# Optimization experiments

Hardware: AMD Instinct MI355X
Metric: run time of the kernel (lower is better)

The kernel has to match this reference:

```python
import jax, jax.numpy as jnp
import numpy as np

D = 256; HEADS = 8; DH = 32; LVLS = 3; PTS = 4; FF = 1024; FCD = 12544
SHAPES = ((100, 152), (50, 76), (25, 38))  # stride 8/16/32 maps for an 800x1216 image
INCH = (512, 1024, 2048)
N = 2; P_IMG = 1000


def sine_pos(h, w):
    # PositionEmbeddingSine, normalize=True, fully-valid mask
    eps = 1e-6; scale = 2.0 * np.pi
    y = jnp.cumsum(jnp.ones((h, w), jnp.float32), 0)
    x = jnp.cumsum(jnp.ones((h, w), jnp.float32), 1)
    y = y / (y[-1:, :] + eps) * scale
    x = x / (x[:, -1:] + eps) * scale
    dim_t = 10000.0 ** ((2.0 * (jnp.arange(128) // 2)).astype(jnp.float32) / 128.0)
    def inter(p):  # interleave sin/cos like torch.stack(...).flatten(3)
        return jnp.stack([jnp.sin(p[..., 0::2]), jnp.cos(p[..., 1::2])], -1).reshape(h, w, 128)
    return jnp.concatenate([inter(y[..., None] / dim_t), inter(x[..., None] / dim_t)], -1).reshape(h * w, D)


def bilinear(img, gx, gy):
    # F.grid_sample bilinear, align_corners=False, padding_mode='zeros'
    # img [C,H,W]; gx,gy in [-1,1] of any shape -> out [C, *gx.shape]
    C, H, W = img.shape
    x = ((gx + 1.0) * W - 1.0) * 0.5
    y = ((gy + 1.0) * H - 1.0) * 0.5
    x0 = jnp.floor(x); y0 = jnp.floor(y)
    wx = x - x0; wy = y - y0
    x0i = x0.astype(jnp.int32); y0i = y0.astype(jnp.int32)
    def g(xi, yi):
        ok = ((xi >= 0) & (xi < W) & (yi >= 0) & (yi < H)).astype(img.dtype)
        v = img[:, jnp.clip(yi, 0, H - 1), jnp.clip(xi, 0, W - 1)]
        return v * ok[None]
    return (g(x0i, y0i) * ((1 - wx) * (1 - wy))[None]
            + g(x0i + 1, y0i) * (wx * (1 - wy))[None]
            + g(x0i, y0i + 1) * ((1 - wx) * wy)[None]
            + g(x0i + 1, y0i + 1) * (wx * wy)[None])


def layernorm(x, g, b):
    mu = x.mean(-1, keepdims=True)
    var = ((x - mu) ** 2).mean(-1, keepdims=True)
    return (x - mu) / jnp.sqrt(var + 1e-5) * g + b


def _forward(feat0, feat1, feat2, point_coords, projw, projb, gng, gnb, level_embed,
             w_off, b_off, w_attn, b_attn, w_val, b_val, w_out, b_out,
             ln1_g, ln1_b, ln2_g, ln2_b, w_ff1, b_ff1, w_ff2, b_ff2, fc_w, fc_b):
    feats = (feat0, feat1, feat2)
    srcs = []; poss = []
    for l in range(LVLS):
        # input_proj: 1x1 conv + GroupNorm(32, 256)
        s = jnp.einsum('nchw,oc->nohw', feats[l], projw[l]) + projb[l][None, :, None, None]
        n, c, h, w = s.shape
        sg = s.reshape(n, 32, c // 32, h, w)
        mu = sg.mean((2, 3, 4), keepdims=True)
        var = ((sg - mu) ** 2).mean((2, 3, 4), keepdims=True)
        s = ((sg - mu) / jnp.sqrt(var + 1e-5)).reshape(n, c, h, w) * gng[l][None, :, None, None] + gnb[l][None, :, None, None]
        srcs.append(s.reshape(n, c, h * w).transpose(0, 2, 1))
        poss.append(sine_pos(h, w)[None] + level_embed[l][None, None, :])
    src = jnp.concatenate(srcs, 1)            # [N, Len, D]
    pos = jnp.concatenate(poss, 1)            # [1, Len, D] broadcast
    # reference points (valid_ratios == 1)
    refs = []
    for (h, w) in SHAPES:
        gy, gx = jnp.meshgrid((jnp.arange(h) + 0.5) / h, (jnp.arange(w) + 0.5) / w, indexing='ij')
        refs.append(jnp.stack([gx.ravel(), gy.ravel()], -1))
    ref = jnp.concatenate(refs, 0)            # [Len, 2] (x, y)
    Lq = src.shape[1]
    q = src + pos
    value = (src @ w_val.T + b_val).reshape(N, Lq, HEADS, DH)
    off = (q @ w_off.T + b_off).reshape(N, Lq, HEADS, LVLS, PTS, 2)
    aw = jax.nn.softmax((q @ w_attn.T + b_attn).reshape(N, Lq, HEADS, LVLS * PTS), -1).reshape(N, Lq, HEADS, LVLS, PTS)
    norm = jnp.array([[w, h] for (h, w) in SHAPES], jnp.float32)  # [L, 2] offset normalizer (W_, H_)
    locs = ref[None, :, None, None, None, :] + off / norm[None, None, None, :, None, :]  # [N,Lq,H,L,P,2]
    # MSDeformAttn core: per-level bilinear gather, accumulate weighted samples
    acc = jnp.zeros((N * HEADS, DH, Lq), src.dtype)
    start = 0
    for lvl, (h, w) in enumerate(SHAPES):
        v = value[:, start:start + h * w].transpose(0, 2, 3, 1).reshape(N * HEADS, DH, h, w)
        g = (2.0 * locs[:, :, :, lvl] - 1.0).transpose(0, 2, 1, 3, 4).reshape(N * HEADS, Lq, PTS, 2)
        s = jax.vmap(bilinear)(v, g[..., 0], g[..., 1])                 # [NH, DH, Lq, PTS]
        a = aw[:, :, :, lvl].transpose(0, 2, 1, 3).reshape(N * HEADS, 1, Lq, PTS)
        acc = acc + (s * a).sum(-1)
        start += h * w
    attn_out = acc.reshape(N, HEADS * DH, Lq).transpose(0, 2, 1) @ w_out.T + b_out
    x = layernorm(src + attn_out, ln1_g, ln1_b)
    ff = jax.nn.relu(x @ w_ff1.T + b_ff1) @ w_ff2.T + b_ff2
    x = layernorm(x + ff, ln2_g, ln2_b)
    # take level-0 tokens back to a feature map
    H0, W0 = SHAPES[0]
    mem = x.transpose(0, 2, 1)[:, :, :H0 * W0].reshape(N, D, H0, W0)
    # point_sample: grid_sample at 2*coords-1
    gpc = 2.0 * point_coords - 1.0
    pf = jax.vmap(bilinear)(mem, gpc[..., 0], gpc[..., 1])              # [N, D, P]
    pf = pf.transpose(0, 2, 1).reshape(N * P_IMG, D)
    # fc: Conv1d(256 -> 12544, k=1) + relu, then squeeze/permute
    return jax.nn.relu(pf @ fc_w.T + fc_b[None])


def setup_inputs() -> dict:
    key = jax.random.key(0)
    ki = iter(jax.random.split(key, 48))
    def rn(shape, scale):
        return jax.random.normal(next(ki), shape, jnp.float32) * scale
    d = {}
    d['feat0'] = jax.random.normal(next(ki), (N, 512, 100, 152), jnp.float32)
    d['feat1'] = jax.random.normal(next(ki), (N, 1024, 50, 76), jnp.float32)
    d['feat2'] = jax.random.normal(next(ki), (N, 2048, 25, 38), jnp.float32)
    d['point_coords'] = jax.random.uniform(next(ki), (N, P_IMG, 2), jnp.float32)
    d['gt_classes'] = jax.random.randint(next(ki), (N * P_IMG,), 0, 81)
    for l in range(LVLS):
        cin = INCH[l]
        d[f'proj{l}_w'] = rn((D, cin), 1.0 / np.sqrt(cin))
        d[f'proj{l}_b'] = jnp.zeros((D,), jnp.float32)
        d[f'gn{l}_g'] = jnp.ones((D,), jnp.float32)
        d[f'gn{l}_b'] = jnp.zeros((D,), jnp.float32)
    d['level_embed'] = rn((LVLS, D), 1.0)
    d['w_off'] = rn((HEADS * LVLS * PTS * 2, D), 0.01)
    d['b_off'] = rn((HEADS * LVLS * PTS * 2,), 0.2)
    d['w_attn'] = rn((HEADS * LVLS * PTS, D), 0.01)
    d['b_attn'] = jnp.zeros((HEADS * LVLS * PTS,), jnp.float32)
    d['w_val'] = rn((D, D), 1.0 / 16)
    d['b_val'] = jnp.zeros((D,), jnp.float32)
    d['w_out'] = rn((D, D), 1.0 / 16)
    d['b_out'] = jnp.zeros((D,), jnp.float32)
    d['ln1_g'] = jnp.ones((D,), jnp.float32); d['ln1_b'] = jnp.zeros((D,), jnp.float32)
    d['ln2_g'] = jnp.ones((D,), jnp.float32); d['ln2_b'] = jnp.zeros((D,), jnp.float32)
    d['w_ff1'] = rn((FF, D), 1.0 / 16); d['b_ff1'] = jnp.zeros((FF,), jnp.float32)
    d['w_ff2'] = rn((D, FF), 1.0 / 32); d['b_ff2'] = jnp.zeros((D,), jnp.float32)
    d['fc_w'] = rn((FCD, D), 1.0 / 16); d['fc_b'] = jnp.zeros((FCD,), jnp.float32)
    return d


def reference(feat0, feat1, feat2, point_coords, gt_classes,
              proj0_w, proj0_b, gn0_g, gn0_b, proj1_w, proj1_b, gn1_g, gn1_b,
              proj2_w, proj2_b, gn2_g, gn2_b, level_embed,
              w_off, b_off, w_attn, b_attn, w_val, b_val, w_out, b_out,
              ln1_g, ln1_b, ln2_g, ln2_b, w_ff1, b_ff1, w_ff2, b_ff2, fc_w, fc_b):
    out = _forward(feat0, feat1, feat2, point_coords,
                   (proj0_w, proj1_w, proj2_w), (proj0_b, proj1_b, proj2_b),
                   (gn0_g, gn1_g, gn2_g), (gn0_b, gn1_b, gn2_b), level_embed,
                   w_off, b_off, w_attn, b_attn, w_val, b_val, w_out, b_out,
                   ln1_g, ln1_b, ln2_g, ln2_b, w_ff1, b_ff1, w_ff2, b_ff2, fc_w, fc_b)
    return (out, gt_classes)
```

## Files before the change

kernel.cpp:

```cpp
#include <hip/hip_runtime.h>
#include <cstddef>
#include <cstdint>

#define D_MODEL 256
#define LQ 19950
#define NBATCH 2
#define NT (NBATCH*LQ)

typedef short  bf16x8 __attribute__((ext_vector_type(8)));
typedef float  f32x4  __attribute__((ext_vector_type(4)));
typedef unsigned short u16x8 __attribute__((ext_vector_type(8)));
typedef unsigned short u16x4 __attribute__((ext_vector_type(4)));
typedef _Float16 h16x2 __attribute__((ext_vector_type(2)));

__device__ __forceinline__ unsigned short f2b(float f) {
  unsigned u = __float_as_uint(f);
  u += 0x7fff + ((u >> 16) & 1);
  return (unsigned short)(u >> 16);
}
__device__ __forceinline__ float b2f(unsigned short s) {
  return __uint_as_float(((unsigned)s) << 16);
}
__device__ __forceinline__ bf16x8 pack8(float4 a, float4 b) {
  bf16x8 r;
  r[0]=(short)f2b(a.x); r[1]=(short)f2b(a.y); r[2]=(short)f2b(a.z); r[3]=(short)f2b(a.w);
  r[4]=(short)f2b(b.x); r[5]=(short)f2b(b.y); r[6]=(short)f2b(b.z); r[7]=(short)f2b(b.w);
  return r;
}

#if __has_builtin(__builtin_amdgcn_global_load_lds)
#define HAVE_GLL 1
__device__ __forceinline__ void gload16(const void* g, void* lds_base_uniform) {
  __builtin_amdgcn_global_load_lds(
      (const __attribute__((address_space(1))) void*)g,
      (__attribute__((address_space(3))) void*)lds_base_uniform, 16, 0, 0);
}
#else
#define HAVE_GLL 0
#endif

template<bool ABF, int BMODE, bool CBF, bool RELU, bool ROWBIAS>
__global__ __launch_bounds__(256) void mgemm(
    const void* __restrict__ Av, const void* __restrict__ Bv,
    const float* __restrict__ bias, void* __restrict__ Cv,
    int M, int N, int K, int lda, int ldb, long sB, long sC, int zShift)
{
  __shared__ unsigned short As[64][72];
  __shared__ unsigned short Bs[64][72];
  const int tid = threadIdx.x;
  const int n0 = blockIdx.x * 64, m0 = blockIdx.y * 64;
  const int zb = blockIdx.z;
  const int n_b = zb >> zShift;
  const int kBase = (zb & ((1 << zShift) - 1)) * K;
  const int lane = tid & 63;
  const int wave = tid >> 6;
  const int l15 = lane & 15, q = lane >> 4;
  const int m_off = (wave >> 1) * 32, n_off = (wave & 1) * 32;
  f32x4 acc[2][2] = {};

  for (int k0 = kBase; k0 < kBase + K; k0 += 64) {
    {
      int row = tid >> 2, kc = (tid & 3) * 8;
      int gm = m0 + row;
      bf16x8 v0 = (bf16x8)0, v1 = (bf16x8)0;
      if (gm < M) {
        if constexpr (ABF) {
          const unsigned short* A = (const unsigned short*)Av;
          v0 = *(const bf16x8*)&A[(size_t)gm*lda + k0 + kc];
          v1 = *(const bf16x8*)&A[(size_t)gm*lda + k0 + kc + 32];
        } else {
          const float* A = (const float*)Av;
          const float* p = &A[(size_t)gm*lda + k0 + kc];
          v0 = pack8(*(const float4*)p,      *(const float4*)(p+4));
          v1 = pack8(*(const float4*)(p+32), *(const float4*)(p+36));
        }
      }
      *(bf16x8*)&As[row][kc]    = v0;
      *(bf16x8*)&As[row][kc+32] = v1;
    }
    if constexpr (BMODE == 1) {
      const float* Bp = (const float*)Bv + (size_t)n_b * sB;
      int kr = tid >> 3, nc = (tid & 7) * 8;
      #pragma unroll
      for (int half = 0; half < 2; ++half) {
        int kk = kr + half*32;
        const float* p = &Bp[(size_t)(k0+kk)*ldb + n0 + nc];
        float v[8];
        if (n0 + nc + 7 < N) {
          float2 a0 = *(const float2*)p,     a1 = *(const float2*)(p+2);
          float2 a2 = *(const float2*)(p+4), a3 = *(const float2*)(p+6);
          v[0]=a0.x; v[1]=a0.y; v[2]=a1.x; v[3]=a1.y;
          v[4]=a2.x; v[5]=a2.y; v[6]=a3.x; v[7]=a3.y;
        } else {
          #pragma unroll
          for (int i=0;i<8;++i) v[i] = (n0+nc+i < N) ? p[i] : 0.f;
        }
        #pragma unroll
        for (int i=0;i<8;++i) Bs[nc+i][kk] = f2b(v[i]);
      }
    }
    __syncthreads();
    #pragma unroll
    for (int s = 0; s < 2; ++s) {
      bf16x8 a0 = *(const bf16x8*)&As[m_off      + l15][s*32 + q*8];
      bf16x8 a1 = *(const bf16x8*)&As[m_off + 16 + l15][s*32 + q*8];
      bf16x8 b0 = *(const bf16x8*)&Bs[n_off      + l15][s*32 + q*8];
      bf16x8 b1 = *(const bf16x8*)&Bs[n_off + 16 + l15][s*32 + q*8];
      acc[0][0] = __builtin_amdgcn_mfma_f32_16x16x32_bf16(a0, b0, acc[0][0], 0,0,0);
      acc[0][1] = __builtin_amdgcn_mfma_f32_16x16x32_bf16(a0, b1, acc[0][1], 0,0,0);
      acc[1][0] = __builtin_amdgcn_mfma_f32_16x16x32_bf16(a1, b0, acc[1][0], 0,0,0);
      acc[1][1] = __builtin_amdgcn_mfma_f32_16x16x32_bf16(a1, b1, acc[1][1], 0,0,0);
    }
    __syncthreads();
  }
  float* Cf = (float*)Cv + (size_t)zb * sC;
  unsigned short* Cb = (unsigned short*)Cv + (size_t)zb * sC;
  #pragma unroll
  for (int r = 0; r < 2; ++r) {
    #pragma unroll
    for (int c = 0; c < 2; ++c) {
      #pragma unroll
      for (int v = 0; v < 4; ++v) {
        int gm = m0 + m_off + r*16 + q*4 + v;
        int gn = n0 + n_off + c*16 + l15;
        if (gm < M && gn < N) {
          float o = acc[r][c][v];
          if (bias) o += ROWBIAS ? bias[gm] : bias[gn];
          if (RELU) o = fmaxf(o, 0.f);
          if constexpr (CBF) Cb[(size_t)gm*N + gn] = f2b(o);
          else               Cf[(size_t)gm*N + gn] = o;
        }
      }
    }
  }
}

__global__ __launch_bounds__(256) void proj_reduce2(
    const float* __restrict__ part, const float* __restrict__ bias,
    float* __restrict__ out, int HW, int S)
{
  int half = HW >> 1;
  int per_n = D_MODEL * half;
  int total = NBATCH * per_n;
  const float2* p2 = (const float2*)part;
  float2* o2 = (float2*)out;
  for (int i = blockIdx.x*256 + threadIdx.x; i < total; i += gridDim.x*256) {
    int n = i / per_n;
    int r = i - n*per_n;
    int o = r / half;
    int hw2 = r - o*half;
    float ax = 0.f, ay = 0.f;
    for (int s = 0; s < S; ++s) {
      float2 v = p2[((size_t)(n*S+s)*D_MODEL + o)*half + hw2];
      ax += v.x; ay += v.y;
    }
    float b = bias[o];
    o2[(size_t)o*HW + (size_t)n*half + hw2] = make_float2(ax+b, ay+b);
  }
}

template<bool CBF, bool RELU, bool RB>
__global__ __launch_bounds__(512) void gemm_bb(
    const unsigned short* __restrict__ A, const unsigned short* __restrict__ B,
    const float* __restrict__ bias, void* __restrict__ Cv,
    int M, int N, int K, int lda, int ldb)
{
  __shared__ unsigned short SA[8192];
  __shared__ unsigned short SB[8192];
  const int tid = threadIdx.x;
  const int lane = tid & 63, wave = tid >> 6;
  const int nwg = gridDim.x * gridDim.y;
  const int flat = blockIdx.y * gridDim.x + blockIdx.x;
  const int qn = nwg >> 3, rr = nwg & 7;
  const int xcd = flat & 7, lid = flat >> 3;
  const int swz = (xcd < rr ? xcd*(qn+1) : rr*(qn+1) + (xcd-rr)*qn) + lid;
  const int n0 = (swz % gridDim.x) * 128;
  const int m0 = (swz / gridDim.x) * 128;

  const int l15 = lane & 15, q = lane >> 4;
  const int m_off = (wave >> 2) * 64, n_off = (wave & 3) * 32;
  const int sr = lane >> 3;
  const int ssl = (lane & 7) ^ sr;
  const int rs = l15 & 7;
  f32x4 acc[4][2] = {};

  for (int k0 = 0; k0 < K; k0 += 64) {
    #pragma unroll
    for (int c = 0; c < 2; ++c) {
      int ch = wave*2 + c;
      const unsigned short* ga = A + (size_t)(m0 + ch*8 + sr)*lda + k0 + ssl*8;
      const unsigned short* gb = B + (size_t)(n0 + ch*8 + sr)*ldb + k0 + ssl*8;
#if HAVE_GLL
      gload16(ga, &SA[ch*512]);
      gload16(gb, &SB[ch*512]);
#else
      *(bf16x8*)&SA[ch*512 + lane*8] = *(const bf16x8*)ga;
      *(bf16x8*)&SB[ch*512 + lane*8] = *(const bf16x8*)gb;
#endif
    }
    __syncthreads();
    #pragma unroll
    for (int s = 0; s < 2; ++s) {
      int ps = ((s*4 + q) ^ rs) * 8;
      bf16x8 af[4], bfr[2];
      #pragma unroll
      for (int i = 0; i < 4; ++i)
        af[i] = *(const bf16x8*)&SA[(m_off + i*16 + l15)*64 + ps];
      #pragma unroll
      for (int j = 0; j < 2; ++j)
        bfr[j] = *(const bf16x8*)&SB[(n_off + j*16 + l15)*64 + ps];
      #pragma unroll
      for (int i = 0; i < 4; ++i)
        #pragma unroll
        for (int j = 0; j < 2; ++j)
          acc[i][j] = __builtin_amdgcn_mfma_f32_16x16x32_bf16(af[i], bfr[j], acc[i][j], 0,0,0);
    }
    __syncthreads();
  }

  float* Cf = (float*)Cv;
  unsigned short* Cb = (unsigned short*)Cv;
  #pragma unroll
  for (int i = 0; i < 4; ++i) {
    #pragma unroll
    for (int j = 0; j < 2; ++j) {
      #pragma unroll
      for (int v = 0; v < 4; ++v) {
        int gm = m0 + m_off + i*16 + q*4 + v;
        int gn = n0 + n_off + j*16 + l15;
        if (gm < M && gn < N) {
          float o = acc[i][j][v];
          if (bias) o += RB ? bias[gm] : bias[gn];
          if (RELU) o = fmaxf(o, 0.f);
          if constexpr (CBF) Cb[(size_t)gm*N + gn] = f2b(o);
          else               Cf[(size_t)gm*N + gn] = o;
        }
      }
    }
  }
}

__global__ __launch_bounds__(512) void gemm_vo(
    const unsigned short* __restrict__ Asrc, const unsigned short* __restrict__ Aq,
    const unsigned short* __restrict__ Bv,   const unsigned short* __restrict__ Bo,
    const float* __restrict__ bias_v, const float* __restrict__ bias_o,
    unsigned short* __restrict__ Cv, unsigned short* __restrict__ Co, int M)
{
  __shared__ unsigned short SA[8192];
  __shared__ unsigned short SB[8192];
  const int tid = threadIdx.x;
  const int lane = tid & 63, wave = tid >> 6;
  const int nwg = gridDim.x * gridDim.y;
  const int flat = blockIdx.y * gridDim.x + blockIdx.x;
  const int qn = nwg >> 3, rr = nwg & 7;
  const int xcd = flat & 7, lid = flat >> 3;
  const int swz = (xcd < rr ? xcd*(qn+1) : rr*(qn+1) + (xcd-rr)*qn) + lid;
  const int colid = swz % gridDim.x;
  const int m0 = (swz / gridDim.x) * 128;

  const unsigned short* A; const unsigned short* B;
  const float* bias; unsigned short* C; int N, n0; bool isv;
  if (colid < 2) { A = Asrc; B = Bv; bias = bias_v; C = Cv; N = 256; n0 = colid*128; isv = true; }
  else           { A = Aq;   B = Bo; bias = bias_o; C = Co; N = 288; n0 = (colid-2)*128; isv = false; }

  const int l15 = lane & 15, q = lane >> 4;
  const int m_off = (wave >> 2) * 64, n_off = (wave & 3) * 32;
  const int sr = lane >> 3;
  const int ssl = (lane & 7) ^ sr;
  const int rs = l15 & 7;
  f32x4 acc[4][2] = {};

  for (int k0 = 0; k0 < 256; k0 += 64) {
    #pragma unroll
    for (int c = 0; c < 2; ++c) {
      int ch = wave*2 + c;
      const unsigned short* ga = A + (size_t)(m0 + ch*8 + sr)*256 + k0 + ssl*8;
      const unsigned short* gb = B + (size_t)(n0 + ch*8 + sr)*256 + k0 + ssl*8;
#if HAVE_GLL
      gload16(ga, &SA[ch*512]);
      gload16(gb, &SB[ch*512]);
#else
      *(bf16x8*)&SA[ch*512 + lane*8] = *(const bf16x8*)ga;
      *(bf16x8*)&SB[ch*512 + lane*8] = *(const bf16x8*)gb;
#endif
    }
    __syncthreads();
    #pragma unroll
    for (int s = 0; s < 2; ++s) {
      int ps = ((s*4 + q) ^ rs) * 8;
      bf16x8 af[4], bfr[2];
      #pragma unroll
      for (int i = 0; i < 4; ++i)
        af[i] = *(const bf16x8*)&SA[(m_off + i*16 + l15)*64 + ps];
      #pragma unroll
      for (int j = 0; j < 2; ++j)
        bfr[j] = *(const bf16x8*)&SB[(n_off + j*16 + l15)*64 + ps];
      #pragma unroll
      for (int i = 0; i < 4; ++i)
        #pragma unroll
        for (int j = 0; j < 2; ++j)
          acc[i][j] = __builtin_amdgcn_mfma_f32_16x16x32_bf16(af[i], bfr[j], acc[i][j], 0,0,0);
    }
    __syncthreads();
  }

  #pragma unroll
  for (int i = 0; i < 4; ++i) {
    #pragma unroll
    for (int j = 0; j < 2; ++j) {
      #pragma unroll
      for (int v = 0; v < 4; ++v) {
        int gm = m0 + m_off + i*16 + q*4 + v;
        int gn = n0 + n_off + j*16 + l15;
        if (gm < M && gn < N) {
          float o = acc[i][j][v] + bias[gn];
          unsigned short bits;
          if (isv) { _Float16 hh = (_Float16)o; bits = *(unsigned short*)&hh; }
          else     { bits = f2b(o); }
          C[(size_t)gm*N + gn] = bits;
        }
      }
    }
  }
}

__global__ __launch_bounds__(256) void tconv(
    const float* __restrict__ feat, unsigned short* __restrict__ featT,
    int C, int HW)
{
  __shared__ float T[32][33];
  int hw0 = blockIdx.x*32, c0 = blockIdx.y*32, n = blockIdx.z;
  const float* base = feat + (size_t)n*C*HW;
  int tx = threadIdx.x & 31, ty = threadIdx.x >> 5;
  #pragma unroll
  for (int it=0; it<4; ++it) {
    int c = c0 + ty + it*8;
    int hw = hw0 + tx;
    T[ty+it*8][tx] = (hw < HW) ? base[(size_t)c*HW + hw] : 0.f;
  }
  __syncthreads();
  #pragma unroll
  for (int it=0; it<4; ++it) {
    int tl = ty + it*8;
    int tok = hw0 + tl;
    if (tok < HW) {
      featT[((size_t)n*HW + tok)*C + c0 + tx] = f2b(T[tx][tl]);
    }
  }
}

struct W9 { const float* src[9]; unsigned short* dst[9]; int nv[9]; };
__global__ __launch_bounds__(256) void wconv(W9 w)
{
  int s = blockIdx.y;
  const float4* src = (const float4*)w.src[s];
  unsigned short* dst = w.dst[s];
  int n = w.nv[s];
  for (int i = blockIdx.x*256 + threadIdx.x; i < n; i += gridDim.x*256) {
    float4 v = src[i];
    u16x4 o = { f2b(v.x), f2b(v.y), f2b(v.z), f2b(v.w) };
    *(u16x4*)(dst + (size_t)i*4) = o;
  }
}

__global__ __launch_bounds__(288) void biascat(
    const float* __restrict__ b_off, const float* __restrict__ b_attn,
    float* __restrict__ out)
{
  int i = threadIdx.x;
  out[i] = (i < 192) ? b_off[i] : b_attn[i - 192];
}

__global__ __launch_bounds__(256) void gn_partial2(
    const float* __restrict__ s2, float* __restrict__ partials, int HW)
{
  int g = blockIdx.x, n = blockIdx.y, c = blockIdx.z;
  int NHW = HW*2;
  int nvec2 = HW >> 1;
  int total = nvec2*8;
  float sum = 0.f, sq = 0.f;
  for (int j = c*256 + threadIdx.x; j < total; j += 2048) {
    int r = j / nvec2;
    int v = j - r*nvec2;
    const float2 x = *(const float2*)(s2 + (size_t)(g*8+r)*NHW + (size_t)n*HW + v*2);
    sum += x.x + x.y;
    sq  += x.x*x.x + x.y*x.y;
  }
  #pragma unroll
  for (int m=32;m;m>>=1){ sum += __shfl_xor(sum,m,64); sq += __shfl_xor(sq,m,64); }
  __shared__ float s1[4], s2s[4];
  int w = threadIdx.x >> 6;
  if ((threadIdx.x & 63) == 0) { s1[w]=sum; s2s[w]=sq; }
  __syncthreads();
  if (threadIdx.x == 0) {
    partials[(((size_t)n*32+g)*8 + c)*2]     = s1[0]+s1[1]+s1[2]+s1[3];
    partials[(((size_t)n*32+g)*8 + c)*2 + 1] = s2s[0]+s2s[1]+s2s[2]+s2s[3];
  }
}

__global__ __launch_bounds__(256) void gn_apply2(
    const float* __restrict__ s2, const float* __restrict__ partials,
    const float* __restrict__ gw, const float* __restrict__ gb,
    float* __restrict__ src, int HW, int loff)
{
  __shared__ float T[32][33];
  __shared__ float smu[4], srs[4];
  int tx = threadIdx.x & 31, ty = threadIdx.x >> 5;
  int hw0 = blockIdx.x*32, o0 = blockIdx.y*32, n = blockIdx.z;
  int NHW = HW*2;
  if (threadIdx.x < 4) {
    int g = (o0 >> 3) + threadIdx.x;
    float S = 0.f, Q = 0.f;
    #pragma unroll
    for (int c = 0; c < 8; ++c) {
      S += partials[(((size_t)n*32+g)*8 + c)*2];
      Q += partials[(((size_t)n*32+g)*8 + c)*2 + 1];
    }
    float inv = 1.f/(float)(8*HW);
    float mu = S*inv;
    float var = Q*inv - mu*mu;
    smu[threadIdx.x] = mu;
    srs[threadIdx.x] = rsqrtf(var + 1e-5f);
  }
  __syncthreads();
  #pragma unroll
  for (int it=0; it<4; ++it) {
    int ol = ty + it*8;
    int o = o0 + ol;
    int hw = hw0 + tx;
    float v = 0.f;
    if (hw < HW) {
      v = (s2[(size_t)o*NHW + (size_t)n*HW + hw] - smu[ol>>3])*srs[ol>>3]*gw[o] + gb[o];
    }
    T[ol][tx] = v;
  }
  __syncthreads();
  #pragma unroll
  for (int it=0; it<4; ++it) {
    int tl = ty + it*8;
    int tok = hw0 + tl;
    if (tok < HW) {
      src[((size_t)n*LQ + loff + tok)*D_MODEL + o0 + tx] = T[tx][tl];
    }
  }
}

__global__ __launch_bounds__(256) void compute_q(
    const float* __restrict__ src, const float* __restrict__ level_embed,
    unsigned short* __restrict__ q, unsigned short* __restrict__ srcbf)
{
  int row = blockIdx.x;
  int d = threadIdx.x;
  int tok = (row >= LQ) ? row - LQ : row;
  int H, W, lvl, i, j;
  if (tok < 15200)      { lvl=0; H=100; W=152; int hw=tok;        i=hw/152; j=hw-i*152; }
  else if (tok < 19000) { lvl=1; H=50;  W=76;  int hw=tok-15200;  i=hw/76;  j=hw-i*76;  }
  else                  { lvl=2; H=25;  W=38;  int hw=tok-19000;  i=hw/38;  j=hw-i*38;  }
  const float TWO_PI = 6.28318530717958647692f;
  float yv = (float)(i+1) / ((float)H + 1e-6f) * TWO_PI;
  float xv = (float)(j+1) / ((float)W + 1e-6f) * TWO_PI;
  int m = (d & 127) >> 1;
  float invt = __expf((float)m * -0.14391156516f);
  float ang = ((d < 128) ? yv : xv) * invt;
  float pe = (d & 1) ? __cosf(ang) : __sinf(ang);
  size_t idx = (size_t)row*D_MODEL + d;
  float sv = src[idx];
  q[idx] = f2b(sv + pe + level_embed[lvl*D_MODEL + d]);
  srcbf[idx] = f2b(sv);
}

__global__ __launch_bounds__(256) void deform_sample(
    const unsigned short* __restrict__ value, const unsigned short* __restrict__ offaw,
    unsigned short* __restrict__ accb)
{
  int idx = blockIdx.x*256 + threadIdx.x;
  if (idx >= NT*8*4) return;
  int quarter = idx & 3;
  int h = (idx >> 2) & 7;
  int row = idx >> 5;
  int n = (row >= LQ) ? 1 : 0;
  int tok = row - n*LQ;

  float bxs0, bxs1, bxs2, bys0, bys1, bys2;
  if (tok < 15200) {
    int ti = tok/152, tj = tok - ti*152;
    float bx = tj + 0.5f, by = ti + 0.5f;
    bxs0 = bx - 0.5f;         bys0 = by - 0.5f;
    bxs1 = bx*0.5f - 0.5f;    bys1 = by*0.5f - 0.5f;
    bxs2 = bx*0.25f - 0.5f;   bys2 = by*0.25f - 0.5f;
  } else if (tok < 19000) {
    int hw = tok - 15200; int ti = hw/76, tj = hw - ti*76;
    float bx = tj + 0.5f, by = ti + 0.5f;
    bxs0 = bx*2.f - 0.5f;     bys0 = by*2.f - 0.5f;
    bxs1 = bx - 0.5f;         bys1 = by - 0.5f;
    bxs2 = bx*0.5f - 0.5f;    bys2 = by*0.5f - 0.5f;
  } else {
    int hw = tok - 19000; int ti = hw/38, tj = hw - ti*38;
    float bx = tj + 0.5f, by = ti + 0.5f;
    bxs0 = bx*4.f - 0.5f;     bys0 = by*4.f - 0.5f;
    bxs1 = bx*2.f - 0.5f;     bys1 = by*2.f - 0.5f;
    bxs2 = bx - 0.5f;         bys2 = by - 0.5f;
  }
  const float bxs[3] = {bxs0, bxs1, bxs2};
  const float bys[3] = {bys0, bys1, bys2};

  const unsigned short* offr = offaw + (size_t)row*288 + h*24;
  const unsigned short* awr  = offaw + (size_t)row*288 + 192 + h*12;
  float off[24];
  {
    u16x8 o0 = *(const u16x8*)offr;
    u16x8 o1 = *(const u16x8*)(offr+8);
    u16x8 o2 = *(const u16x8*)(offr+16);
    #pragma unroll
    for (int c=0;c<8;++c){ off[c]=b2f(o0[c]); off[8+c]=b2f(o1[c]); off[16+c]=b2f(o2[c]); }
  }
  float lg[12];
  {
    u16x4 a0 = *(const u16x4*)awr;
    u16x4 a1 = *(const u16x4*)(awr+4);
    u16x4 a2 = *(const u16x4*)(awr+8);
    #pragma unroll
    for (int c=0;c<4;++c){ lg[c]=b2f(a0[c]); lg[4+c]=b2f(a1[c]); lg[8+c]=b2f(a2[c]); }
  }
  float mx = -1e30f;
  #pragma unroll
  for (int i=0;i<12;++i) mx = fmaxf(mx, lg[i]);
  float ssum = 0.f;
  #pragma unroll
  for (int i=0;i<12;++i){ lg[i] = __expf(lg[i]-mx); ssum += lg[i]; }
  float sinv = 1.f/ssum;

  h16x2 acc2[4] = {};
  const int HH[3]={100,50,25}, WW[3]={152,76,38}, OO[3]={0,15200,19000};
  int chbase = h*32 + quarter*8;
  const _Float16* vhalf = (const _Float16*)value;
  #pragma unroll
  for (int lvl=0; lvl<3; ++lvl) {
    const int H=HH[lvl], W=WW[lvl], lo=OO[lvl];
    const _Float16* vbase = vhalf + ((size_t)(n*LQ + lo)*D_MODEL) + chbase;
    #pragma unroll
    for (int p=0; p<4; ++p) {
      float ox = off[lvl*8 + p*2];
      float oy = off[lvl*8 + p*2 + 1];
      float a  = lg[lvl*4 + p] * sinv;
      float x = bxs[lvl] + ox;
      float y = bys[lvl] + oy;
      float x0f = floorf(x), y0f = floorf(y);
      float wx = x - x0f, wy = y - y0f;
      int x0 = (int)x0f, y0 = (int)y0f;
      float w00 = (1.f-wx)*(1.f-wy)*a, w10 = wx*(1.f-wy)*a;
      float w01 = (1.f-wx)*wy*a,       w11 = wx*wy*a;
      if ((unsigned)x0 < (unsigned)(W-1) && (unsigned)y0 < (unsigned)(H-1)) {
        const h16x2* p00 = (const h16x2*)(vbase + (size_t)(y0*W + x0)*D_MODEL);
        const h16x2* p10 = (const h16x2*)(vbase + (size_t)(y0*W + x0 + 1)*D_MODEL);
        const h16x2* p01 = (const h16x2*)(vbase + (size_t)((y0+1)*W + x0)*D_MODEL);
        const h16x2* p11 = (const h16x2*)(vbase + (size_t)((y0+1)*W + x0 + 1)*D_MODEL);
        _Float16 h00 = (_Float16)w00, h10 = (_Float16)w10;
        _Float16 h01 = (_Float16)w01, h11 = (_Float16)w11;
        h16x2 wp00 = {h00,h00}, wp10 = {h10,h10}, wp01 = {h01,h01}, wp11 = {h11,h11};
        #pragma unroll
        for (int k=0;k<4;++k) {
          acc2[k] += wp00*p00[k];
          acc2[k] += wp10*p10[k];
          acc2[k] += wp01*p01[k];
          acc2[k] += wp11*p11[k];
        }
      } else {
        float tw[4] = { w00, w10, w01, w11 };
        #pragma unroll
        for (int t=0; t<4; ++t) {
          int xi = x0 + (t & 1), yi = y0 + (t >> 1);
          if (xi >= 0 && xi < W && yi >= 0 && yi < H) {
            _Float16 wh = (_Float16)tw[t];
            h16x2 wp = {wh, wh};
            const h16x2* vr = (const h16x2*)(vbase + (size_t)(yi*W + xi)*D_MODEL);
            #pragma unroll
            for (int k=0;k<4;++k) acc2[k] += wp*vr[k];
          }
        }
      }
    }
  }
  unsigned short* o = accb + (size_t)row*D_MODEL + chbase;
  u16x8 ov;
  #pragma unroll
  for (int k=0;k<4;++k) {
    ov[k*2]   = f2b((float)acc2[k][0]);
    ov[k*2+1] = f2b((float)acc2[k][1]);
  }
  *(u16x8*)o = ov;
}

template<bool EMITBF>
__global__ __launch_bounds__(256) void ln_add(
    const float* __restrict__ A, const float* __restrict__ B,
    const float* __restrict__ g, const float* __restrict__ b,
    float* __restrict__ out, unsigned short* __restrict__ outbf, int rows)
{
  int wid = (blockIdx.x * 256 + threadIdx.x) >> 6;
  int lane = threadIdx.x & 63;
  if (wid >= rows) return;
  size_t base = (size_t)wid * D_MODEL;
  float4 va = *(const float4*)&A[base + lane*4];
  float4 vb = *(const float4*)&B[base + lane*4];
  float v[4] = {va.x+vb.x, va.y+vb.y, va.z+vb.z, va.w+vb.w};
  float s = v[0]+v[1]+v[2]+v[3];
  #pragma unroll
  for (int m=32; m; m>>=1) s += __shfl_xor(s, m, 64);
  float mu = s * (1.f/256.f);
  float qq = 0.f;
  #pragma unroll
  for (int i=0;i<4;++i){ float d=v[i]-mu; qq += d*d; }
  #pragma unroll
  for (int m=32; m; m>>=1) qq += __shfl_xor(qq, m, 64);
  float rstd = rsqrtf(qq*(1.f/256.f) + 1e-5f);
  float o[4];
  #pragma unroll
  for (int i=0;i<4;++i){
    int d = lane*4+i;
    o[i] = (v[i]-mu)*rstd*g[d] + b[d];
  }
  *(float4*)&out[base + lane*4] = make_float4(o[0],o[1],o[2],o[3]);
  if constexpr (EMITBF) {
    u16x4 ob = { f2b(o[0]), f2b(o[1]), f2b(o[2]), f2b(o[3]) };
    *(u16x4*)&outbf[base + lane*4] = ob;
  }
}

__global__ __launch_bounds__(256) void point_sample(
    const float* __restrict__ x2, const float* __restrict__ pc,
    unsigned short* __restrict__ pf)
{
  int pidx = blockIdx.x;
  int n = pidx / 1000;
  float px = pc[(size_t)pidx*2], py = pc[(size_t)pidx*2+1];
  float x = ((2.f*px)*152.f - 1.f)*0.5f;
  float y = ((2.f*py)*100.f - 1.f)*0.5f;
  float x0f=floorf(x), y0f=floorf(y);
  float wx=x-x0f, wy=y-y0f;
  int x0=(int)x0f, y0=(int)y0f;
  int d = threadIdx.x;
  float accv = 0.f;
  #pragma unroll
  for (int t=0;t<4;++t) {
    int xi = x0 + (t&1), yi = y0 + (t>>1);
    float w = ((t&1)?wx:(1.f-wx)) * ((t>>1)?wy:(1.f-wy));
    if (xi>=0 && xi<152 && yi>=0 && yi<100) {
      accv += w * x2[((size_t)(n*LQ + yi*152 + xi))*D_MODEL + d];
    }
  }
  pf[(size_t)pidx*D_MODEL + d] = f2b(accv);
}

__global__ void copy_gt(const int* __restrict__ gt, float* __restrict__ out, int nels)
{
  int i = blockIdx.x*256 + threadIdx.x;
  if (i < nels) out[i] = (float)gt[i];
}

extern "C" void kernel_launch(void* const* d_in, const int* in_sizes, int n_in,
                              void* d_out, int out_size, void* d_ws, size_t ws_size,
                              hipStream_t stream)
{
  const float* feat[3]  = {(const float*)d_in[0], (const float*)d_in[1], (const float*)d_in[2]};
  const float* pc       = (const float*)d_in[3];
  const int*   gt       = (const int*)d_in[4];
  const float* projw[3] = {(const float*)d_in[5],  (const float*)d_in[9],  (const float*)d_in[13]};
  const float* projb[3] = {(const float*)d_in[6],  (const float*)d_in[10], (const float*)d_in[14]};
  const float* gng[3]   = {(const float*)d_in[7],  (const float*)d_in[11], (const float*)d_in[15]};
  const float* gnb[3]   = {(const float*)d_in[8],  (const float*)d_in[12], (const float*)d_in[16]};
  const float* level_embed = (const float*)d_in[17];
  const float* w_off  = (const float*)d_in[18];
  const float* b_off  = (const float*)d_in[19];
  const float* w_attn = (const float*)d_in[20];
  const float* b_attn = (const float*)d_in[21];
  const float* w_val  = (const float*)d_in[22];
  const float* b_val  = (const float*)d_in[23];
  const float* w_out  = (const float*)d_in[24];
  const float* b_out  = (const float*)d_in[25];
  const float* ln1g   = (const float*)d_in[26];
  const float* ln1b   = (const float*)d_in[27];
  const float* ln2g   = (const float*)d_in[28];
  const float* ln2b   = (const float*)d_in[29];
  const float* wff1   = (const float*)d_in[30];
  const float* bff1   = (const float*)d_in[31];
  const float* wff2   = (const float*)d_in[32];
  const float* bff2   = (const float*)d_in[33];
  const float* fcw    = (const float*)d_in[34];
  const float* fcb    = (const float*)d_in[35];

  float* ws    = (float*)d_ws;
  float* s_tmp = ws;
  unsigned short* q_b     = (unsigned short*)(s_tmp + 10214400);
  unsigned short* value_b = q_b + 10214400;
  float* srcb  = (float*)(value_b + 10214400);
  float* xreg  = srcb + 10214400;
  unsigned short* offaw   = (unsigned short*)(xreg + 10214400);
  unsigned short* wbf     = offaw + 11491200;
  float* partials = (float*)(wbf + 4333568);
  float* boffaw   = partials + 1024;

  unsigned short* wv_bf  = wbf;
  unsigned short* wof_bf = wbf + 65536;
  unsigned short* wat_bf = wbf + 114688;
  unsigned short* wou_bf = wbf + 139264;
  unsigned short* wf1_bf = wbf + 204800;
  unsigned short* wf2_bf = wbf + 466944;
  unsigned short* wfc_bf = wbf + 729088;
  unsigned short* wp0_bf = wbf + 3940352;
  unsigned short* wp1_bf = wbf + 4071424;

  unsigned short* featT = q_b;
  float* kpart = xreg;
  unsigned short* src_bf = (unsigned short*)xreg;
  unsigned short* acc_b = q_b;
  unsigned short* xb_bf = offaw;
  unsigned short* hbuf  = (unsigned short*)s_tmp;
  unsigned short* pf    = value_b;
  float* ybuf = srcb;
  float* x2   = s_tmp;

  W9 w9;
  w9.src[0]=w_val;    w9.dst[0]=wv_bf;  w9.nv[0]=65536/4;
  w9.src[1]=w_off;    w9.dst[1]=wof_bf; w9.nv[1]=49152/4;
  w9.src[2]=w_attn;   w9.dst[2]=wat_bf; w9.nv[2]=24576/4;
  w9.src[3]=w_out;    w9.dst[3]=wou_bf; w9.nv[3]=65536/4;
  w9.src[4]=wff1;     w9.dst[4]=wf1_bf; w9.nv[4]=262144/4;
  w9.src[5]=wff2;     w9.dst[5]=wf2_bf; w9.nv[5]=262144/4;
  w9.src[6]=fcw;      w9.dst[6]=wfc_bf; w9.nv[6]=3211264/4;
  w9.src[7]=projw[0]; w9.dst[7]=wp0_bf; w9.nv[7]=131072/4;
  w9.src[8]=projw[1]; w9.dst[8]=wp1_bf; w9.nv[8]=262144/4;
  wconv<<<dim3(512, 9), 256, 0, stream>>>(w9);
  biascat<<<1, 288, 0, stream>>>(b_off, b_attn, boffaw);

  {
    tconv<<<dim3(475, 16, 2), 256, 0, stream>>>(feat[0], featT, 512, 15200);
    gemm_bb<false,false,true><<<dim3(238, 2), 512, 0, stream>>>(
        wp0_bf, featT, projb[0], s_tmp, 256, 30400, 512, 512, 512);
    gn_partial2<<<dim3(32, 2, 8), 256, 0, stream>>>(s_tmp, partials, 15200);
    gn_apply2<<<dim3(475, 8, 2), 256, 0, stream>>>(
        s_tmp, partials, gng[0], gnb[0], srcb, 15200, 0);
  }
  {
    tconv<<<dim3(119, 32, 2), 256, 0, stream>>>(feat[1], featT, 1024, 3800);
    gemm_bb<false,false,true><<<dim3(60, 2), 512, 0, stream>>>(
        wp1_bf, featT, projb[1], s_tmp, 256, 7600, 1024, 1024, 1024);
    gn_partial2<<<dim3(32, 2, 8), 256, 0, stream>>>(s_tmp, partials, 3800);
    gn_apply2<<<dim3(119, 8, 2), 256, 0, stream>>>(
        s_tmp, partials, gng[1], gnb[1], srcb, 3800, 15200);
  }
  {
    mgemm<false,1,false,false,true><<<dim3(15, 4, 8), 256, 0, stream>>>(
        projw[2], feat[2], nullptr, kpart, D_MODEL, 950, 512, 2048, 950,
        (long)2048*950, (long)D_MODEL*950, 2);
    int total2 = NBATCH * D_MODEL * (950 >> 1);
    int gr = (total2 + 255) / 256; if (gr > 2048) gr = 2048;
    proj_reduce2<<<gr, 256, 0, stream>>>(kpart, projb[2], s_tmp, 950, 4);
    gn_partial2<<<dim3(32, 2, 8), 256, 0, stream>>>(s_tmp, partials, 950);
    gn_apply2<<<dim3(30, 8, 2), 256, 0, stream>>>(
        s_tmp, partials, gng[2], gnb[2], srcb, 950, 19000);
  }

  compute_q<<<NT, 256, 0, stream>>>(srcb, level_embed, q_b, src_bf);

  int gm128 = (NT + 127) / 128;
  gemm_vo<<<dim3(5, gm128), 512, 0, stream>>>(
      src_bf, q_b, wv_bf, wof_bf, b_val, boffaw, value_b, offaw, NT);

  deform_sample<<<(NT*8*4 + 255)/256, 256, 0, stream>>>(value_b, offaw, acc_b);

  gemm_bb<false,false,false><<<dim3(2, gm128), 512, 0, stream>>>(
      acc_b, wou_bf, b_out, s_tmp, NT, 256, 256, 256, 256);
  ln_add<true><<<(NT+3)/4, 256, 0, stream>>>(srcb, s_tmp, ln1g, ln1b, xreg, xb_bf, NT);

  gemm_bb<true,true,false><<<dim3(8, gm128), 512, 0, stream>>>(
      xb_bf, wf1_bf, bff1, hbuf, NT, 1024, 256, 256, 256);
  gemm_bb<false,false,false><<<dim3(2, gm128), 512, 0, stream>>>(
      hbuf, wf2_bf, bff2, ybuf, NT, 256, 1024, 1024, 1024);

  ln_add<false><<<(NT+3)/4, 256, 0, stream>>>(xreg, ybuf, ln2g, ln2b, x2, nullptr, NT);

  point_sample<<<2000, 256, 0, stream>>>(x2, pc, pf);
  gemm_bb<false,true,false><<<dim3(12544/128, (2000+127)/128), 512, 0, stream>>>(
      pf, wfc_bf, fcb, (float*)d_out, 2000, 12544, 256, 256, 256);
  copy_gt<<<8, 256, 0, stream>>>(gt, (float*)d_out + (size_t)2000*12544, 2000);
}
```

Measured before the change: 460.8 us.

## Fuse positional query build into GroupNorm apply and add 128x256 GEMM tiles

Removes the separate compute_q kernel: gn_apply2 now also writes the bf16 copy of src and the bf16 query (src plus sine positional embedding plus level embedding). That avoids re-reading the fp32 src buffer in a second pass. It also adds gemm_wide, which uses 128x256 output tiles (4x4 MFMA accumulators per wave) for the input projections, FFN1 and the final FC. This halves the grid and improves operand reuse, at the cost of more registers and shared memory per block and fewer workgroups in flight. The k-partial scratch buffer moves to offaw to avoid aliasing with src_bf, which now lives in xreg and is written earlier.

```diff
diff --git a/kernel.cpp b/kernel.cpp
--- a/kernel.cpp
+++ b/kernel.cpp
@@ -240,6 +240,94 @@
   }
 }
 
+template<bool CBF, bool RELU, bool RB>
+__global__ __launch_bounds__(512) void gemm_wide(
+    const unsigned short* __restrict__ A, const unsigned short* __restrict__ B,
+    const float* __restrict__ bias, void* __restrict__ Cv,
+    int M, int N, int K, int lda, int ldb)
+{
+  __shared__ unsigned short SA[8192];
+  __shared__ unsigned short SB[16384];
+  const int tid = threadIdx.x;
+  const int lane = tid & 63, wave = tid >> 6;
+  const int nwg = gridDim.x * gridDim.y;
+  const int flat = blockIdx.y * gridDim.x + blockIdx.x;
+  const int qn = nwg >> 3, rr = nwg & 7;
+  const int xcd = flat & 7, lid = flat >> 3;
+  const int swz = (xcd < rr ? xcd*(qn+1) : rr*(qn+1) + (xcd-rr)*qn) + lid;
+  const int n0 = (swz % gridDim.x) * 256;
+  const int m0 = (swz / gridDim.x) * 128;
+
+  const int l15 = lane & 15, q = lane >> 4;
+  const int m_off = (wave >> 2) * 64, n_off = (wave & 3) * 64;
+  const int sr = lane >> 3;
+  const int ssl = (lane & 7) ^ sr;
+  const int rs = l15 & 7;
+  f32x4 acc[4][4] = {};
+
+  for (int k0 = 0; k0 < K; k0 += 64) {
+    #pragma unroll
+    for (int c = 0; c < 2; ++c) {
+      int ch = wave*2 + c;
+      const unsigned short* ga = A + (size_t)(m0 + ch*8 + sr)*lda + k0 + ssl*8;
+#if HAVE_GLL
+      gload16(ga, &SA[ch*512]);
+#else
+      *(bf16x8*)&SA[ch*512 + lane*8] = *(const bf16x8*)ga;
+#endif
+    }
+    #pragma unroll
+    for (int c = 0; c < 4; ++c) {
+      int ch = wave*4 + c;
+      const unsigned short* gb = B + (size_t)(n0 + ch*8 + sr)*ldb + k0 + ssl*8;
+#if HAVE_GLL
+      gload16(gb, &SB[ch*512]);
+#else
+      *(bf16x8*)&SB[ch*512 + lane*8] = *(const bf16x8*)gb;
+#endif
+    }
+    __syncthreads();
+    #pragma unroll
+    for (int s = 0; s < 2; ++s) {
+      int ps = ((s*4 + q) ^ rs) * 8;
+      bf16x8 af[4], bfr[4];
+      #pragma unroll
+      for (int i = 0; i < 4; ++i)
+        af[i] = *(const bf16x8*)&SA[(m_off + i*16 + l15)*64 + ps];
+      #pragma unroll
+      for (int j = 0; j < 4; ++j)
+        bfr[j] = *(const bf16x8*)&SB[(n_off + j*16 + l15)*64 + ps];
+      #pragma unroll
+      for (int i = 0; i < 4; ++i)
+        #pragma unroll
+        for (int j = 0; j < 4; ++j)
+          acc[i][j] = __builtin_amdgcn_mfma_f32_16x16x32_bf16(af[i], bfr[j], acc[i][j], 0,0,0);
+    }
+    __syncthreads();
+  }
+
+  float* Cf = (float*)Cv;
+  unsigned short* Cb = (unsigned short*)Cv;
+  #pragma unroll
+  for (int i = 0; i < 4; ++i) {
+    #pragma unroll
+    for (int j = 0; j < 4; ++j) {
+      #pragma unroll
+      for (int v = 0; v < 4; ++v) {
+        int gm = m0 + m_off + i*16 + q*4 + v;
+        int gn = n0 + n_off + j*16 + l15;
+        if (gm < M && gn < N) {
+          float o = acc[i][j][v];
+          if (bias) o += RB ? bias[gm] : bias[gn];
+          if (RELU) o = fmaxf(o, 0.f);
+          if constexpr (CBF) Cb[(size_t)gm*N + gn] = f2b(o);
+          else               Cf[(size_t)gm*N + gn] = o;
+        }
+      }
+    }
+  }
+}
+
 __global__ __launch_bounds__(512) void gemm_vo(
     const unsigned short* __restrict__ Asrc, const unsigned short* __restrict__ Aq,
     const unsigned short* __restrict__ Bv,   const unsigned short* __restrict__ Bo,
@@ -401,7 +489,10 @@
 __global__ __launch_bounds__(256) void gn_apply2(
     const float* __restrict__ s2, const float* __restrict__ partials,
     const float* __restrict__ gw, const float* __restrict__ gb,
-    float* __restrict__ src, int HW, int loff)
+    const float* __restrict__ le,
+    float* __restrict__ src, unsigned short* __restrict__ srcbf,
+    unsigned short* __restrict__ qb,
+    int HW, int loff, int W, float invW, float invH2pi, float invW2pi)
 {
   __shared__ float T[32][33];
   __shared__ float smu[4], srs[4];
@@ -435,38 +526,26 @@
     T[ol][tx] = v;
   }
   __syncthreads();
+  int d = o0 + tx;
+  int m = (d & 127) >> 1;
+  float invt = __expf((float)m * -0.14391156516f);
+  float lev  = le[d];
   #pragma unroll
   for (int it=0; it<4; ++it) {
     int tl = ty + it*8;
     int tok = hw0 + tl;
     if (tok < HW) {
-      src[((size_t)n*LQ + loff + tok)*D_MODEL + o0 + tx] = T[tx][tl];
-    }
-  }
-}
-
-__global__ __launch_bounds__(256) void compute_q(
-    const float* __restrict__ src, const float* __restrict__ level_embed,
-    unsigned short* __restrict__ q, unsigned short* __restrict__ srcbf)
-{
-  int row = blockIdx.x;
-  int d = threadIdx.x;
-  int tok = (row >= LQ) ? row - LQ : row;
-  int H, W, lvl, i, j;
-  if (tok < 15200)      { lvl=0; H=100; W=152; int hw=tok;        i=hw/152; j=hw-i*152; }
-  else if (tok < 19000) { lvl=1; H=50;  W=76;  int hw=tok-15200;  i=hw/76;  j=hw-i*76;  }
-  else                  { lvl=2; H=25;  W=38;  int hw=tok-19000;  i=hw/38;  j=hw-i*38;  }
-  const float TWO_PI = 6.28318530717958647692f;
-  float yv = (float)(i+1) / ((float)H + 1e-6f) * TWO_PI;
-  float xv = (float)(j+1) / ((float)W + 1e-6f) * TWO_PI;
-  int m = (d & 127) >> 1;
-  float invt = __expf((float)m * -0.14391156516f);
-  float ang = ((d < 128) ? yv : xv) * invt;
-  float pe = (d & 1) ? __cosf(ang) : __sinf(ang);
-  size_t idx = (size_t)row*D_MODEL + d;
-  float sv = src[idx];
-  q[idx] = f2b(sv + pe + level_embed[lvl*D_MODEL + d]);
-  srcbf[idx] = f2b(sv);
+      size_t idx = ((size_t)n*LQ + loff + tok)*D_MODEL + d;
+      float v = T[tx][tl];
+      src[idx] = v;
+      srcbf[idx] = f2b(v);
+      int i = __float2int_rd(((float)tok + 0.5f) * invW);
+      int j = tok - i*W;
+      float ang = ((d < 128) ? (float)(i+1)*invH2pi : (float)(j+1)*invW2pi) * invt;
+      float pe = (d & 1) ? __cosf(ang) : __sinf(ang);
+      qb[idx] = f2b(v + pe + lev);
+    }
+  }
 }
 
 __global__ __launch_bounds__(256) void deform_sample(
@@ -711,7 +790,7 @@
   unsigned short* wp1_bf = wbf + 4071424;
 
   unsigned short* featT = q_b;
-  float* kpart = xreg;
+  float* kpart = (float*)offaw;
   unsigned short* src_bf = (unsigned short*)xreg;
   unsigned short* acc_b = q_b;
   unsigned short* xb_bf = offaw;
@@ -733,21 +812,24 @@
   wconv<<<dim3(512, 9), 256, 0, stream>>>(w9);
   biascat<<<1, 288, 0, stream>>>(b_off, b_attn, boffaw);
 
+  const float PI2 = 6.28318530717958647692f;
   {
     tconv<<<dim3(475, 16, 2), 256, 0, stream>>>(feat[0], featT, 512, 15200);
-    gemm_bb<false,false,true><<<dim3(238, 2), 512, 0, stream>>>(
+    gemm_wide<false,false,true><<<dim3(119, 2), 512, 0, stream>>>(
         wp0_bf, featT, projb[0], s_tmp, 256, 30400, 512, 512, 512);
     gn_partial2<<<dim3(32, 2, 8), 256, 0, stream>>>(s_tmp, partials, 15200);
     gn_apply2<<<dim3(475, 8, 2), 256, 0, stream>>>(
-        s_tmp, partials, gng[0], gnb[0], srcb, 15200, 0);
+        s_tmp, partials, gng[0], gnb[0], level_embed, srcb, src_bf, q_b,
+        15200, 0, 152, 1.0f/152.f, PI2/(100.f+1e-6f), PI2/(152.f+1e-6f));
   }
   {
     tconv<<<dim3(119, 32, 2), 256, 0, stream>>>(feat[1], featT, 1024, 3800);
-    gemm_bb<false,false,true><<<dim3(60, 2), 512, 0, stream>>>(
+    gemm_wide<false,false,true><<<dim3(30, 2), 512, 0, stream>>>(
         wp1_bf, featT, projb[1], s_tmp, 256, 7600, 1024, 1024, 1024);
     gn_partial2<<<dim3(32, 2, 8), 256, 0, stream>>>(s_tmp, partials, 3800);
     gn_apply2<<<dim3(119, 8, 2), 256, 0, stream>>>(
-        s_tmp, partials, gng[1], gnb[1], srcb, 3800, 15200);
+        s_tmp, partials, gng[1], gnb[1], level_embed + 256, srcb, src_bf, q_b,
+        3800, 15200, 76, 1.0f/76.f, PI2/(50.f+1e-6f), PI2/(76.f+1e-6f));
   }
   {
     mgemm<false,1,false,false,true><<<dim3(15, 4, 8), 256, 0, stream>>>(
@@ -758,10 +840,9 @@
     proj_reduce2<<<gr, 256, 0, stream>>>(kpart, projb[2], s_tmp, 950, 4);
     gn_partial2<<<dim3(32, 2, 8), 256, 0, stream>>>(s_tmp, partials, 950);
     gn_apply2<<<dim3(30, 8, 2), 256, 0, stream>>>(
-        s_tmp, partials, gng[2], gnb[2], srcb, 950, 19000);
-  }
-
-  compute_q<<<NT, 256, 0, stream>>>(srcb, level_embed, q_b, src_bf);
+        s_tmp, partials, gng[2], gnb[2], level_embed + 512, srcb, src_bf, q_b,
+        950, 19000, 38, 1.0f/38.f, PI2/(25.f+1e-6f), PI2/(38.f+1e-6f));
+  }
 
   int gm128 = (NT + 127) / 128;
   gemm_vo<<<dim3(5, gm128), 512, 0, stream>>>(
@@ -773,7 +854,7 @@
       acc_b, wou_bf, b_out, s_tmp, NT, 256, 256, 256, 256);
   ln_add<true><<<(NT+3)/4, 256, 0, stream>>>(srcb, s_tmp, ln1g, ln1b, xreg, xb_bf, NT);
 
-  gemm_bb<true,true,false><<<dim3(8, gm128), 512, 0, stream>>>(
+  gemm_wide<true,true,false><<<dim3(4, gm128), 512, 0, stream>>>(
       xb_bf, wf1_bf, bff1, hbuf, NT, 1024, 256, 256, 256);
   gemm_bb<false,false,false><<<dim3(2, gm128), 512, 0, stream>>>(
       hbuf, wf2_bf, bff2, ybuf, NT, 256, 1024, 1024, 1024);
@@ -781,7 +862,7 @@
   ln_add<false><<<(NT+3)/4, 256, 0, stream>>>(xreg, ybuf, ln2g, ln2b, x2, nullptr, NT);
 
   point_sample<<<2000, 256, 0, stream>>>(x2, pc, pf);
-  gemm_bb<false,true,false><<<dim3(12544/128, (2000+127)/128), 512, 0, stream>>>(
+  gemm_wide<false,true,false><<<dim3(49, (2000+127)/128), 512, 0, stream>>>(
       pf, wfc_bf, fcb, (float*)d_out, 2000, 12544, 256, 256, 256);
   copy_gt<<<8, 256, 0, stream>>>(gt, (float*)d_out + (size_t)2000*12544, 2000);
 }
```

Result: slower. 480.7 us (+4.3%).
